# Kernel optimization log

Hardware: AMD Instinct MI355X
Metric: run time of the kernel (lower is better)

Reference implementation:

```python
import jax, jax.numpy as jnp
import numpy as np
import math

D_MODEL = 512
N_HEAD = 8
HEAD_DIM = D_MODEL // N_HEAD


def _rel_sinusoid(seq_len, dim):
    # Sinusoidal embedding for relative positions -seq_len .. seq_len-1, shape [2L, dim]
    half = dim // 2
    inv_freq = jnp.exp(jnp.arange(half, dtype=jnp.float32) * (-math.log(10000.0) / (half - 1)))
    ang = jnp.arange(-seq_len, seq_len, dtype=jnp.float32)[:, None] * inv_freq[None, :]
    return jnp.concatenate([jnp.sin(ang), jnp.cos(ang)], axis=1)  # [2L, dim]


def _shift(BD):
    # Transformer-XL shift trick: [b, n, L, 2L] -> [b, n, L, L]
    b, n, L, _ = BD.shape
    BD = jnp.concatenate([BD, jnp.zeros((b, n, L, 1), BD.dtype)], axis=-1)  # [b,n,L,2L+1]
    BD = BD.reshape(b, n, -1, L)[:, :, :-1].reshape(b, n, L, -1)  # [b,n,L,2L]
    return BD[:, :, :, L:]


def setup_inputs() -> dict:
    key = jax.random.key(0)
    ks = jax.random.split(key, 6)
    B, L = 8, 1024
    x = jax.random.normal(ks[0], (B, L, D_MODEL), jnp.float32)
    mask = jax.random.randint(ks[1], (B, L), 0, 2).astype(jnp.int32)
    W_qkv = jax.random.normal(ks[2], (D_MODEL, 3 * D_MODEL), jnp.float32) / math.sqrt(D_MODEL)
    r_r_bias = jax.random.normal(ks[3], (N_HEAD, HEAD_DIM), jnp.float32) * 0.1
    r_w_bias = jax.random.normal(ks[4], (N_HEAD, HEAD_DIM), jnp.float32) * 0.1
    w_kr = jax.random.normal(ks[5], (HEAD_DIM, HEAD_DIM), jnp.float32) * 0.1
    return {"x": x, "mask": mask, "W_qkv": W_qkv, "r_r_bias": r_r_bias, "r_w_bias": r_w_bias, "w_kr": w_kr}


def reference(x, mask, W_qkv, r_r_bias, r_w_bias, w_kr):
    B, L, d_model = x.shape
    scale = math.sqrt(HEAD_DIM)
    pos_embed = _rel_sinusoid(L, HEAD_DIM)  # [2L, head_dim]

    qkv = x @ W_qkv  # [B, L, 3*d_model]
    q, k, v = jnp.split(qkv, 3, axis=-1)
    q = q.reshape(B, L, N_HEAD, HEAD_DIM).transpose(0, 2, 1, 3)  # [B, H, L, hd]
    k = k.reshape(B, L, N_HEAD, HEAD_DIM).transpose(0, 2, 1, 3)
    v = v.reshape(B, L, N_HEAD, HEAD_DIM).transpose(0, 2, 1, 3)

    rw_head_q = q + r_r_bias[None, :, None, :]
    AC = jnp.einsum('bnqd,bnkd->bnqk', rw_head_q, k)  # [B,H,L,L]

    rel = pos_embed @ w_kr  # [2L, hd]
    D_ = jnp.einsum('nd,ld->nl', r_w_bias, rel)[None, :, None, :]  # [1,H,1,2L]
    B_ = jnp.einsum('bnqd,ld->bnql', q, rel)  # [B,H,L,2L]
    BD = _shift(B_ + D_)  # [B,H,L,L]

    attn = (AC + BD) / scale
    attn = jnp.where(mask[:, None, None, :] == 0, jnp.float32(1e-9), attn)
    attn = jax.nn.softmax(attn, axis=-1)  # dropout is identity at eval

    out = jnp.einsum('bnqk,bnkd->bnqd', attn, v)  # [B,H,L,hd]
    return out.transpose(0, 2, 1, 3).reshape(B, L, d_model)
```

## Files before the change

kernel.cpp:

```cpp
#include <hip/hip_runtime.h>
#include <hip/hip_bf16.h>
#include <stdint.h>

typedef __bf16 bf16x8 __attribute__((ext_vector_type(8)));
typedef float  f32x4  __attribute__((ext_vector_type(4)));

#define D_MODEL 512
#define N_HEAD  8
#define HD      64
#define L_      1024
#define SCALE   0.125f
#define EXP_NEG8 3.35462628e-4f
#define L2E     1.44269504f
#define NEG8L2E -11.54156036f

__device__ __forceinline__ unsigned short f2bf(float f) {
  unsigned int u = __builtin_bit_cast(unsigned int, f);
  u += 0x7FFFu + ((u >> 16) & 1u);
  return (unsigned short)(u >> 16);
}
__device__ __forceinline__ float bf2f(unsigned short h) {
  unsigned int u = ((unsigned int)h) << 16;
  return __builtin_bit_cast(float, u);
}

__device__ __forceinline__ void gld_lds16(const void* g, void* l) {
  __builtin_amdgcn_global_load_lds(
      (const __attribute__((address_space(1))) void*)g,
      (__attribute__((address_space(3))) void*)l, 16, 0, 0);
}
__device__ __forceinline__ void gld_lds4(const void* g, void* l) {
  __builtin_amdgcn_global_load_lds(
      (const __attribute__((address_space(1))) void*)g,
      (__attribute__((address_space(3))) void*)l, 4, 0, 0);
}

__global__ __launch_bounds__(256) void k_cvt_x(const float* __restrict__ x,
                                               unsigned short* __restrict__ xbf) {
  int t = blockIdx.x * 256 + threadIdx.x;
  const float4* p = reinterpret_cast<const float4*>(x) + (size_t)t * 2;
  float4 a = p[0], b = p[1];
  ushort4 o0 = { f2bf(a.x), f2bf(a.y), f2bf(a.z), f2bf(a.w) };
  ushort4 o1 = { f2bf(b.x), f2bf(b.y), f2bf(b.z), f2bf(b.w) };
  ushort4* q = reinterpret_cast<ushort4*>(xbf) + (size_t)t * 2;
  q[0] = o0; q[1] = o1;
}

__global__ __launch_bounds__(256) void k_cvt_wt(const float* __restrict__ W,
                                                unsigned short* __restrict__ Wt) {
  __shared__ float tile[32][33];
  int kb = blockIdx.x;
  int nb = blockIdx.y;
  int t = threadIdx.x;
  int r = t >> 3, c4 = (t & 7) * 4;
  float4 v = *reinterpret_cast<const float4*>(W + (size_t)(kb * 32 + r) * 1536 + nb * 32 + c4);
  tile[r][c4 + 0] = v.x; tile[r][c4 + 1] = v.y; tile[r][c4 + 2] = v.z; tile[r][c4 + 3] = v.w;
  __syncthreads();
  int a = t >> 3, b4 = (t & 7) * 4;
  ushort4 o = { f2bf(tile[b4 + 0][a]), f2bf(tile[b4 + 1][a]),
                f2bf(tile[b4 + 2][a]), f2bf(tile[b4 + 3][a]) };
  *reinterpret_cast<ushort4*>(Wt + (size_t)(nb * 32 + a) * 512 + kb * 32 + b4) = o;
}

__global__ __launch_bounds__(256) void k_stab(float* __restrict__ SCF,
                                              unsigned short* __restrict__ SBF) {
  int tid = blockIdx.x * 256 + threadIdx.x;
  int l = tid >> 6, d = tid & 63;
  const float kInv = -9.210340371976184f / 31.0f;
  float f = expf((float)(d & 31) * kInv);
  float ang = (float)l * f;
  float v = (d < 32) ? sinf(ang) : cosf(ang);
  SCF[tid] = v;
  SBF[tid] = f2bf(v);
}

__global__ __launch_bounds__(256, 3) void k_gemm_qkv(const unsigned short* __restrict__ Xbf,
                                                     const unsigned short* __restrict__ Wt,
                                                     const float* __restrict__ rrb,
                                                     unsigned short* __restrict__ QKV,
                                                     unsigned short* __restrict__ Vt) {
  __shared__ unsigned short As[2][128][32];
  __shared__ unsigned short Bs[2][128][32];
  int lin = blockIdx.y * 64 + blockIdx.x;
  int xcd = lin & 7, idx = lin >> 3;
  int bx = xcd * 8 + idx / 12;
  int by = idx % 12;
  int m0 = bx * 128;
  int n0 = by * 128;
  int w = threadIdx.x >> 6, lane = threadIdx.x & 63;
  int lr = lane & 15, g = lane >> 4;
  int wm = (w >> 1) * 64, wn = (w & 1) * 64;
  int srow = lane >> 2, schk = (lane & 3) * 8;

  auto stage = [&](int buf, int k0) {
#pragma unroll
    for (int j = 0; j < 2; ++j) {
      int row = w * 32 + j * 16 + srow;
      gld_lds16(Xbf + (size_t)(m0 + row) * 512 + k0 + schk, &As[buf][w * 32 + j * 16][0]);
      gld_lds16(Wt  + (size_t)(n0 + row) * 512 + k0 + schk, &Bs[buf][w * 32 + j * 16][0]);
    }
  };

  f32x4 acc[4][4];
  for (int i = 0; i < 4; ++i) for (int j = 0; j < 4; ++j) acc[i][j] = (f32x4){0.f, 0.f, 0.f, 0.f};

  stage(0, 0);
  __syncthreads();

  for (int it = 0; it < 16; ++it) {
    int cur = it & 1;
    if (it < 15) stage(cur ^ 1, (it + 1) * 32);
    bf16x8 a[4], b[4];
#pragma unroll
    for (int mt = 0; mt < 4; ++mt)
      a[mt] = __builtin_bit_cast(bf16x8, *reinterpret_cast<const uint4*>(&As[cur][wm + mt * 16 + lr][g * 8]));
#pragma unroll
    for (int nt = 0; nt < 4; ++nt)
      b[nt] = __builtin_bit_cast(bf16x8, *reinterpret_cast<const uint4*>(&Bs[cur][wn + nt * 16 + lr][g * 8]));
#pragma unroll
    for (int mt = 0; mt < 4; ++mt)
#pragma unroll
      for (int nt = 0; nt < 4; ++nt)
        acc[mt][nt] = __builtin_amdgcn_mfma_f32_16x16x32_bf16(a[mt], b[nt], acc[mt][nt], 0, 0, 0);
    __syncthreads();
  }

  int region = n0 >> 9;
  if (region == 2) {
#pragma unroll
    for (int mt = 0; mt < 4; ++mt)
#pragma unroll
      for (int nt = 0; nt < 4; ++nt) {
        int m = m0 + wm + mt * 16 + g * 4;
        int n = n0 + wn + nt * 16 + lr;
        int nv = n - 1024;
        int bb = m >> 10, h = nv >> 6, d = nv & 63;
        ushort4 o = { f2bf(acc[mt][nt][0]), f2bf(acc[mt][nt][1]),
                      f2bf(acc[mt][nt][2]), f2bf(acc[mt][nt][3]) };
        *reinterpret_cast<ushort4*>(Vt + (size_t)((bb * 8 + h) * 64 + d) * 1024 + (m & 1023)) = o;
      }
  } else if (region == 0) {
#pragma unroll
    for (int mt = 0; mt < 4; ++mt)
#pragma unroll
      for (int nt = 0; nt < 4; ++nt) {
        int n = n0 + wn + nt * 16 + lr;
        float bias = rrb[n];
#pragma unroll
        for (int r = 0; r < 4; ++r) {
          int m = m0 + wm + mt * 16 + g * 4 + r;
          QKV[(size_t)m * 1536 + n] = f2bf((acc[mt][nt][r] + bias) * SCALE);
        }
      }
  } else {
#pragma unroll
    for (int mt = 0; mt < 4; ++mt)
#pragma unroll
      for (int nt = 0; nt < 4; ++nt)
#pragma unroll
        for (int r = 0; r < 4; ++r) {
          int m = m0 + wm + mt * 16 + g * 4 + r;
          int n = n0 + wn + nt * 16 + lr;
          QKV[(size_t)m * 1536 + n] = f2bf(acc[mt][nt][r]);
        }
  }
}

__global__ __launch_bounds__(256) void k_aq(const unsigned short* __restrict__ QKV,
                                            const float* __restrict__ wkr,
                                            const float* __restrict__ rrb,
                                            const float* __restrict__ rwb,
                                            const float* __restrict__ SCF,
                                            unsigned short* __restrict__ Aq) {
  __shared__ float wkrS[64][65];
  __shared__ float qS[64][65];
  __shared__ float zS[64][65];
  int blk = blockIdx.x;
  int bh = blk >> 4, lt = blk & 15;
  int b = bh >> 3, h = bh & 7;
  int t = threadIdx.x;
  for (int idx = t; idx < 4096; idx += 256) wkrS[idx >> 6][idx & 63] = wkr[idx];
  {
    int r = t >> 2, c0 = (t & 3) * 16;
    const unsigned short* qp = QKV + (size_t)(b * L_ + lt * 64 + r) * 1536 + h * HD;
    for (int jj = 0; jj < 16; ++jj) {
      int d = c0 + jj;
      qS[r][d] = bf2f(qp[d]) * 8.f - rrb[h * HD + d] + rwb[h * HD + d];
    }
  }
  __syncthreads();
  {
    int r = t >> 2, e0 = (t & 3) * 16;
    float acc[16];
    for (int ii = 0; ii < 16; ++ii) acc[ii] = 0.f;
    for (int d = 0; d < 64; ++d) {
      float qv = qS[r][d];
      for (int ii = 0; ii < 16; ++ii) acc[ii] += wkrS[e0 + ii][d] * qv;
    }
    for (int ii = 0; ii < 16; ++ii) zS[r][e0 + ii] = acc[ii];
  }
  __syncthreads();
  {
    int r = t >> 2, d0 = (t & 3) * 16;
    int pos = lt * 64 + r;
    const float* sc = SCF + (size_t)pos * 64;
    unsigned short* ap = Aq + ((size_t)bh * L_ + lt * 64 + r) * 64;
    for (int jj = 0; jj < 16; ++jj) {
      int d = d0 + jj;
      float a;
      if (d < 32) a = zS[r][d] * sc[d + 32] + zS[r][d + 32] * sc[d];
      else        a = zS[r][d] * sc[d]      - zS[r][d - 32] * sc[d - 32];
      ap[d] = f2bf(a * SCALE);
    }
  }
}

__global__ __launch_bounds__(256, 2) void k_attn(const unsigned short* __restrict__ QKV,
                                                 const unsigned short* __restrict__ Vt,
                                                 const unsigned short* __restrict__ Sbf,
                                                 const unsigned short* __restrict__ Aq,
                                                 const int* __restrict__ mask,
                                                 float* __restrict__ out) {
  __shared__ unsigned short KtS[2][64][64];
  __shared__ unsigned short VtS[2][64][64];
  __shared__ unsigned short SbS[2][64][64];
  __shared__ int MtS[2][64];
  __shared__ unsigned short pS[4][32][64];

  int n_ = blockIdx.x;
  int l = (n_ & 7) * 64 + (n_ >> 3);
  int bh = l >> 3, qt = l & 7;
  int b = bh >> 3, h = bh & 7;
  int w = threadIdx.x >> 6, lane = threadIdx.x & 63;
  int lr = lane & 15, g = lane >> 4;
  int qw0 = qt * 128 + w * 32;
  int rsub = lane >> 3;
  int csub = (lane & 7) ^ rsub;
  int swz = lr & 7;

  bf16x8 qrr[2][2], qa[2][2];
#pragma unroll
  for (int mt = 0; mt < 2; ++mt) {
    const unsigned short* qrow = QKV + (size_t)(b * L_ + qw0 + mt * 16 + lr) * 1536 + h * HD;
    const unsigned short* arow = Aq + ((size_t)bh * L_ + qw0 + mt * 16 + lr) * HD;
#pragma unroll
    for (int ks = 0; ks < 2; ++ks) {
      qrr[mt][ks] = __builtin_bit_cast(bf16x8, *reinterpret_cast<const uint4*>(qrow + ks * 32 + g * 8));
      qa[mt][ks]  = __builtin_bit_cast(bf16x8, *reinterpret_cast<const uint4*>(arow + ks * 32 + g * 8));
    }
  }

  auto stage = [&](int nb, int k0n) {
#pragma unroll
    for (int j = 0; j < 2; ++j) {
      int row = w * 16 + j * 8;
      const unsigned short* gK = QKV + (size_t)(b * L_ + k0n + row + rsub) * 1536 +
                                 D_MODEL + h * HD + csub * 8;
      gld_lds16(gK, &KtS[nb][row][0]);
      const unsigned short* gV = Vt + (size_t)(bh * HD + row + rsub) * L_ + k0n + csub * 8;
      gld_lds16(gV, &VtS[nb][row][0]);
      const unsigned short* gS = Sbf + (size_t)(k0n + row + rsub) * HD + csub * 8;
      gld_lds16(gS, &SbS[nb][row][0]);
    }
    if (w == 0) gld_lds4(mask + b * L_ + k0n + lane, &MtS[nb][0]);
  };

  stage(0, 0);

  float lsum[2] = {0.f, 0.f};
  f32x4 accO[2][4];
#pragma unroll
  for (int mt = 0; mt < 2; ++mt)
#pragma unroll
    for (int nt = 0; nt < 4; ++nt) accO[mt][nt] = (f32x4){0.f, 0.f, 0.f, 0.f};

  char* psw = (char*)&pS[w][0][0];
  __syncthreads();

  for (int it = 0; it < 16; ++it) {
    int k0 = it << 6;
    int cur = it & 1;
    if (it < 15) stage(cur ^ 1, k0 + 64);

    f32x4 ac[2][4];
#pragma unroll
    for (int mt = 0; mt < 2; ++mt)
#pragma unroll
      for (int t4 = 0; t4 < 4; ++t4) ac[mt][t4] = (f32x4){0.f, 0.f, 0.f, 0.f};
#pragma unroll
    for (int t4 = 0; t4 < 4; ++t4) {
#pragma unroll
      for (int ks = 0; ks < 2; ++ks) {
        const unsigned short* kp = &KtS[cur][t4 * 16 + lr][((((ks << 2) | g) ^ swz) << 3)];
        bf16x8 kfr = __builtin_bit_cast(bf16x8, *reinterpret_cast<const uint4*>(kp));
        ac[0][t4] = __builtin_amdgcn_mfma_f32_16x16x32_bf16(kfr, qrr[0][ks], ac[0][t4], 0, 0, 0);
        ac[1][t4] = __builtin_amdgcn_mfma_f32_16x16x32_bf16(kfr, qrr[1][ks], ac[1][t4], 0, 0, 0);
      }
#pragma unroll
      for (int ks = 0; ks < 2; ++ks) {
        const unsigned short* sp = &SbS[cur][t4 * 16 + lr][((((ks << 2) | g) ^ swz) << 3)];
        bf16x8 sfr = __builtin_bit_cast(bf16x8, *reinterpret_cast<const uint4*>(sp));
        ac[0][t4] = __builtin_amdgcn_mfma_f32_16x16x32_bf16(sfr, qa[0][ks], ac[0][t4], 0, 0, 0);
        ac[1][t4] = __builtin_amdgcn_mfma_f32_16x16x32_bf16(sfr, qa[1][ks], ac[1][t4], 0, 0, 0);
      }
    }

#pragma unroll
    for (int t4 = 0; t4 < 4; ++t4) {
      int4 mk = *reinterpret_cast<const int4*>(&MtS[cur][t4 * 16 + g * 4]);
#pragma unroll
      for (int mt = 0; mt < 2; ++mt) {
        float e0 = __builtin_amdgcn_exp2f(fmaf(ac[mt][t4][0], L2E, NEG8L2E));
        float e1 = __builtin_amdgcn_exp2f(fmaf(ac[mt][t4][1], L2E, NEG8L2E));
        float e2 = __builtin_amdgcn_exp2f(fmaf(ac[mt][t4][2], L2E, NEG8L2E));
        float e3 = __builtin_amdgcn_exp2f(fmaf(ac[mt][t4][3], L2E, NEG8L2E));
        e0 = mk.x ? e0 : EXP_NEG8;
        e1 = mk.y ? e1 : EXP_NEG8;
        e2 = mk.z ? e2 : EXP_NEG8;
        e3 = mk.w ? e3 : EXP_NEG8;
        lsum[mt] += (e0 + e1) + (e2 + e3);
        unsigned int lo, hi;
        asm("v_cvt_pk_bf16_f32 %0, %1, %2" : "=v"(lo) : "v"(e0), "v"(e1));
        asm("v_cvt_pk_bf16_f32 %0, %1, %2" : "=v"(hi) : "v"(e2), "v"(e3));
        uint2 pk; pk.x = lo; pk.y = hi;
        *reinterpret_cast<uint2*>(psw + ((mt * 16 + lr) * 128 +
            (((t4 << 5) | (g << 3)) ^ (swz << 4)))) = pk;
      }
    }

    bf16x8 pa[2][2];
#pragma unroll
    for (int mt = 0; mt < 2; ++mt)
#pragma unroll
      for (int ks = 0; ks < 2; ++ks)
        pa[mt][ks] = __builtin_bit_cast(bf16x8, *reinterpret_cast<const uint4*>(
            psw + ((mt * 16 + lr) * 128 + (((ks << 6) | (g << 4)) ^ (swz << 4)))));
#pragma unroll
    for (int nt = 0; nt < 4; ++nt)
#pragma unroll
      for (int ks = 0; ks < 2; ++ks) {
        const unsigned short* vp = &VtS[cur][nt * 16 + lr][((((ks << 2) | g) ^ swz) << 3)];
        bf16x8 vfr = __builtin_bit_cast(bf16x8, *reinterpret_cast<const uint4*>(vp));
        accO[0][nt] = __builtin_amdgcn_mfma_f32_16x16x32_bf16(pa[0][ks], vfr, accO[0][nt], 0, 0, 0);
        accO[1][nt] = __builtin_amdgcn_mfma_f32_16x16x32_bf16(pa[1][ks], vfr, accO[1][nt], 0, 0, 0);
      }
    __syncthreads();
  }

#pragma unroll
  for (int mt = 0; mt < 2; ++mt) {
    lsum[mt] += __shfl_xor(lsum[mt], 16);
    lsum[mt] += __shfl_xor(lsum[mt], 32);
  }
  float dsum[2][4];
#pragma unroll
  for (int mt = 0; mt < 2; ++mt)
#pragma unroll
    for (int r = 0; r < 4; ++r) dsum[mt][r] = __shfl(lsum[mt], g * 4 + r);

#pragma unroll
  for (int mt = 0; mt < 2; ++mt)
#pragma unroll
    for (int nt = 0; nt < 4; ++nt)
#pragma unroll
      for (int r = 0; r < 4; ++r) {
        int q = qw0 + mt * 16 + g * 4 + r;
        out[(size_t)(b * L_ + q) * D_MODEL + h * HD + nt * 16 + lr] = accO[mt][nt][r] / dsum[mt][r];
      }
}

extern "C" void kernel_launch(void* const* d_in, const int* in_sizes, int n_in,
                              void* d_out, int out_size, void* d_ws, size_t ws_size,
                              hipStream_t stream) {
  const float* x    = (const float*)d_in[0];
  const int*   mask = (const int*)d_in[1];
  const float* Wqkv = (const float*)d_in[2];
  const float* rrb  = (const float*)d_in[3];
  const float* rwb  = (const float*)d_in[4];
  const float* wkr  = (const float*)d_in[5];
  float* out = (float*)d_out;

  char* ws = (char*)d_ws;
  size_t off = 0;
  unsigned short* XBF = (unsigned short*)(ws + off); off += (size_t)8192 * 512 * 2;
  unsigned short* WT  = (unsigned short*)(ws + off); off += (size_t)1536 * 512 * 2;
  unsigned short* QKV = (unsigned short*)(ws + off); off += (size_t)8192 * 1536 * 2;
  unsigned short* VT  = (unsigned short*)(ws + off); off += (size_t)64 * 64 * 1024 * 2;
  float*          SCF = (float*)(ws + off);          off += (size_t)1024 * 64 * 4;
  unsigned short* SBF = (unsigned short*)(ws + off); off += (size_t)1024 * 64 * 2;
  unsigned short* AQ  = XBF;

  hipLaunchKernelGGL(k_cvt_x,    dim3(2048),   dim3(256), 0, stream, x, XBF);
  hipLaunchKernelGGL(k_cvt_wt,   dim3(16, 48), dim3(256), 0, stream, Wqkv, WT);
  hipLaunchKernelGGL(k_stab,     dim3(256),    dim3(256), 0, stream, SCF, SBF);
  hipLaunchKernelGGL(k_gemm_qkv, dim3(64, 12), dim3(256), 0, stream, XBF, WT, rrb, QKV, VT);
  hipLaunchKernelGGL(k_aq,       dim3(1024),   dim3(256), 0, stream, QKV, wkr, rrb, rwb, SCF, AQ);
  hipLaunchKernelGGL(k_attn,     dim3(512),    dim3(256), 0, stream, QKV, VT, SBF, AQ, mask, out);
}
```

Baseline: 113.8 us.

## Fold w_kr projection into QKV GEMM and drop separate Aq kernel

Precomputes W_q·w_kr as extra weight columns, plus a constant from r_w_bias. The QKV GEMM then produces the rotated Aq directly in an added N-region epilogue, which removes the k_aq kernel and its reread of Q. The attention kernel also stops staging the sinusoid table through LDS and loads it straight from global into registers, so the occupancy hint can rise to 3 blocks. The GEMM grows by a third in N, and the sinusoid loads are now unstaged global reads inside the loop.

```diff
diff --git a/kernel.cpp b/kernel.cpp
--- a/kernel.cpp
+++ b/kernel.cpp
@@ -74,17 +74,56 @@
   SBF[tid] = f2bf(v);
 }
 
+__global__ __launch_bounds__(256) void k_wz(const unsigned short* __restrict__ Wt,
+                                            const float* __restrict__ wkr,
+                                            const float* __restrict__ rwb,
+                                            unsigned short* __restrict__ Wzt,
+                                            float* __restrict__ CZ) {
+  __shared__ float wkrS[64][64];
+  __shared__ float panS[64][36];
+  int blk = blockIdx.x;
+  int h = blk >> 4, kc = blk & 15;
+  int t = threadIdx.x;
+  for (int i = t; i < 4096; i += 256) wkrS[i >> 6][i & 63] = wkr[i];
+  {
+    int d = t >> 2, j0 = (t & 3) * 8;
+    const unsigned short* src = Wt + (size_t)(h * 64 + d) * 512 + kc * 32 + j0;
+    for (int j = 0; j < 8; ++j) panS[d][j0 + j] = bf2f(src[j]);
+  }
+  __syncthreads();
+  int e = t >> 2, j0 = (t & 3) * 8;
+  float acc[8];
+  for (int j = 0; j < 8; ++j) acc[j] = 0.f;
+  for (int d = 0; d < 64; ++d) {
+    float wv = wkrS[e][d];
+    for (int j = 0; j < 8; ++j) acc[j] += wv * panS[d][j0 + j];
+  }
+  unsigned short* dst = Wzt + (size_t)(h * 64 + e) * 512 + kc * 32 + j0;
+  ushort4 o0 = { f2bf(acc[0]), f2bf(acc[1]), f2bf(acc[2]), f2bf(acc[3]) };
+  ushort4 o1 = { f2bf(acc[4]), f2bf(acc[5]), f2bf(acc[6]), f2bf(acc[7]) };
+  *reinterpret_cast<ushort4*>(dst) = o0;
+  *reinterpret_cast<ushort4*>(dst + 4) = o1;
+  if (kc == 0 && t < 64) {
+    float c = 0.f;
+    for (int d = 0; d < 64; ++d) c += wkrS[t][d] * rwb[h * 64 + d];
+    CZ[h * 64 + t] = c;
+  }
+}
+
 __global__ __launch_bounds__(256, 3) void k_gemm_qkv(const unsigned short* __restrict__ Xbf,
                                                      const unsigned short* __restrict__ Wt,
                                                      const float* __restrict__ rrb,
+                                                     const float* __restrict__ SCF,
+                                                     const float* __restrict__ CZ,
                                                      unsigned short* __restrict__ QKV,
-                                                     unsigned short* __restrict__ Vt) {
+                                                     unsigned short* __restrict__ Vt,
+                                                     unsigned short* __restrict__ Aq) {
   __shared__ unsigned short As[2][128][32];
   __shared__ unsigned short Bs[2][128][32];
   int lin = blockIdx.y * 64 + blockIdx.x;
   int xcd = lin & 7, idx = lin >> 3;
-  int bx = xcd * 8 + idx / 12;
-  int by = idx % 12;
+  int bx = xcd * 8 + idx / 16;
+  int by = idx % 16;
   int m0 = bx * 128;
   int n0 = by * 128;
   int w = threadIdx.x >> 6, lane = threadIdx.x & 63;
@@ -126,7 +165,33 @@
   }
 
   int region = n0 >> 9;
-  if (region == 2) {
+  if (region == 3) {
+    int nvb = (n0 - 1536) + wn;
+    int h = nvb >> 6;
+    int bb = m0 >> 10;
+    float cz0 = CZ[nvb + lr];
+    float cz1 = CZ[nvb + 16 + lr];
+    float cz2 = CZ[nvb + 32 + lr];
+    float cz3 = CZ[nvb + 48 + lr];
+#pragma unroll
+    for (int mt = 0; mt < 4; ++mt)
+#pragma unroll
+      for (int r = 0; r < 4; ++r) {
+        int m = m0 + wm + mt * 16 + g * 4 + r;
+        int lrow = m & 1023;
+        const float* sc = SCF + (size_t)lrow * 64;
+        float s0 = sc[lr], s1 = sc[16 + lr], c0 = sc[32 + lr], c1 = sc[48 + lr];
+        float z0 = acc[mt][0][r] + cz0;
+        float z1 = acc[mt][1][r] + cz1;
+        float z2 = acc[mt][2][r] + cz2;
+        float z3 = acc[mt][3][r] + cz3;
+        unsigned short* ap = Aq + ((size_t)(bb * 8 + h) * 1024 + lrow) * 64;
+        ap[lr]      = f2bf((z0 * c0 + z2 * s0) * SCALE);
+        ap[16 + lr] = f2bf((z1 * c1 + z3 * s1) * SCALE);
+        ap[32 + lr] = f2bf((z2 * c0 - z0 * s0) * SCALE);
+        ap[48 + lr] = f2bf((z3 * c1 - z1 * s1) * SCALE);
+      }
+  } else if (region == 2) {
 #pragma unroll
     for (int mt = 0; mt < 4; ++mt)
 #pragma unroll
@@ -166,56 +231,7 @@
   }
 }
 
-__global__ __launch_bounds__(256) void k_aq(const unsigned short* __restrict__ QKV,
-                                            const float* __restrict__ wkr,
-                                            const float* __restrict__ rrb,
-                                            const float* __restrict__ rwb,
-                                            const float* __restrict__ SCF,
-                                            unsigned short* __restrict__ Aq) {
-  __shared__ float wkrS[64][65];
-  __shared__ float qS[64][65];
-  __shared__ float zS[64][65];
-  int blk = blockIdx.x;
-  int bh = blk >> 4, lt = blk & 15;
-  int b = bh >> 3, h = bh & 7;
-  int t = threadIdx.x;
-  for (int idx = t; idx < 4096; idx += 256) wkrS[idx >> 6][idx & 63] = wkr[idx];
-  {
-    int r = t >> 2, c0 = (t & 3) * 16;
-    const unsigned short* qp = QKV + (size_t)(b * L_ + lt * 64 + r) * 1536 + h * HD;
-    for (int jj = 0; jj < 16; ++jj) {
-      int d = c0 + jj;
-      qS[r][d] = bf2f(qp[d]) * 8.f - rrb[h * HD + d] + rwb[h * HD + d];
-    }
-  }
-  __syncthreads();
-  {
-    int r = t >> 2, e0 = (t & 3) * 16;
-    float acc[16];
-    for (int ii = 0; ii < 16; ++ii) acc[ii] = 0.f;
-    for (int d = 0; d < 64; ++d) {
-      float qv = qS[r][d];
-      for (int ii = 0; ii < 16; ++ii) acc[ii] += wkrS[e0 + ii][d] * qv;
-    }
-    for (int ii = 0; ii < 16; ++ii) zS[r][e0 + ii] = acc[ii];
-  }
-  __syncthreads();
-  {
-    int r = t >> 2, d0 = (t & 3) * 16;
-    int pos = lt * 64 + r;
-    const float* sc = SCF + (size_t)pos * 64;
-    unsigned short* ap = Aq + ((size_t)bh * L_ + lt * 64 + r) * 64;
-    for (int jj = 0; jj < 16; ++jj) {
-      int d = d0 + jj;
-      float a;
-      if (d < 32) a = zS[r][d] * sc[d + 32] + zS[r][d + 32] * sc[d];
-      else        a = zS[r][d] * sc[d]      - zS[r][d - 32] * sc[d - 32];
-      ap[d] = f2bf(a * SCALE);
-    }
-  }
-}
-
-__global__ __launch_bounds__(256, 2) void k_attn(const unsigned short* __restrict__ QKV,
+__global__ __launch_bounds__(256, 3) void k_attn(const unsigned short* __restrict__ QKV,
                                                  const unsigned short* __restrict__ Vt,
                                                  const unsigned short* __restrict__ Sbf,
                                                  const unsigned short* __restrict__ Aq,
@@ -223,7 +239,6 @@
                                                  float* __restrict__ out) {
   __shared__ unsigned short KtS[2][64][64];
   __shared__ unsigned short VtS[2][64][64];
-  __shared__ unsigned short SbS[2][64][64];
   __shared__ int MtS[2][64];
   __shared__ unsigned short pS[4][32][64];
 
@@ -259,8 +274,6 @@
       gld_lds16(gK, &KtS[nb][row][0]);
       const unsigned short* gV = Vt + (size_t)(bh * HD + row + rsub) * L_ + k0n + csub * 8;
       gld_lds16(gV, &VtS[nb][row][0]);
-      const unsigned short* gS = Sbf + (size_t)(k0n + row + rsub) * HD + csub * 8;
-      gld_lds16(gS, &SbS[nb][row][0]);
     }
     if (w == 0) gld_lds4(mask + b * L_ + k0n + lane, &MtS[nb][0]);
   };
@@ -281,6 +294,14 @@
     int k0 = it << 6;
     int cur = it & 1;
     if (it < 15) stage(cur ^ 1, k0 + 64);
+
+    bf16x8 sf[4][2];
+#pragma unroll
+    for (int t4 = 0; t4 < 4; ++t4)
+#pragma unroll
+      for (int ks = 0; ks < 2; ++ks)
+        sf[t4][ks] = __builtin_bit_cast(bf16x8, *reinterpret_cast<const uint4*>(
+            Sbf + (size_t)(k0 + t4 * 16 + lr) * HD + ks * 32 + g * 8));
 
     f32x4 ac[2][4];
 #pragma unroll
@@ -298,10 +319,8 @@
       }
 #pragma unroll
       for (int ks = 0; ks < 2; ++ks) {
-        const unsigned short* sp = &SbS[cur][t4 * 16 + lr][((((ks << 2) | g) ^ swz) << 3)];
-        bf16x8 sfr = __builtin_bit_cast(bf16x8, *reinterpret_cast<const uint4*>(sp));
-        ac[0][t4] = __builtin_amdgcn_mfma_f32_16x16x32_bf16(sfr, qa[0][ks], ac[0][t4], 0, 0, 0);
-        ac[1][t4] = __builtin_amdgcn_mfma_f32_16x16x32_bf16(sfr, qa[1][ks], ac[1][t4], 0, 0, 0);
+        ac[0][t4] = __builtin_amdgcn_mfma_f32_16x16x32_bf16(sf[t4][ks], qa[0][ks], ac[0][t4], 0, 0, 0);
+        ac[1][t4] = __builtin_amdgcn_mfma_f32_16x16x32_bf16(sf[t4][ks], qa[1][ks], ac[1][t4], 0, 0, 0);
       }
     }
 
@@ -383,17 +402,18 @@
   char* ws = (char*)d_ws;
   size_t off = 0;
   unsigned short* XBF = (unsigned short*)(ws + off); off += (size_t)8192 * 512 * 2;
-  unsigned short* WT  = (unsigned short*)(ws + off); off += (size_t)1536 * 512 * 2;
+  unsigned short* WT  = (unsigned short*)(ws + off); off += (size_t)2048 * 512 * 2;
   unsigned short* QKV = (unsigned short*)(ws + off); off += (size_t)8192 * 1536 * 2;
   unsigned short* VT  = (unsigned short*)(ws + off); off += (size_t)64 * 64 * 1024 * 2;
+  unsigned short* AQ  = (unsigned short*)(ws + off); off += (size_t)64 * 1024 * 64 * 2;
   float*          SCF = (float*)(ws + off);          off += (size_t)1024 * 64 * 4;
   unsigned short* SBF = (unsigned short*)(ws + off); off += (size_t)1024 * 64 * 2;
-  unsigned short* AQ  = XBF;
+  float*          CZ  = (float*)(ws + off);          off += 512 * 4;
 
   hipLaunchKernelGGL(k_cvt_x,    dim3(2048),   dim3(256), 0, stream, x, XBF);
   hipLaunchKernelGGL(k_cvt_wt,   dim3(16, 48), dim3(256), 0, stream, Wqkv, WT);
   hipLaunchKernelGGL(k_stab,     dim3(256),    dim3(256), 0, stream, SCF, SBF);
-  hipLaunchKernelGGL(k_gemm_qkv, dim3(64, 12), dim3(256), 0, stream, XBF, WT, rrb, QKV, VT);
-  hipLaunchKernelGGL(k_aq,       dim3(1024),   dim3(256), 0, stream, QKV, wkr, rrb, rwb, SCF, AQ);
+  hipLaunchKernelGGL(k_wz,       dim3(128),    dim3(256), 0, stream, WT, wkr, rwb, WT + (size_t)1536 * 512, CZ);
+  hipLaunchKernelGGL(k_gemm_qkv, dim3(64, 16), dim3(256), 0, stream, XBF, WT, rrb, SCF, CZ, QKV, VT, AQ);
   hipLaunchKernelGGL(k_attn,     dim3(512),    dim3(256), 0, stream, QKV, VT, SBF, AQ, mask, out);
 }
```

After: 92.75 us. -18.5%, faster.
